# Kernel tuning notes

Hardware: AMD Instinct MI355X
Metric: run time of the kernel (lower is better)

The kernel has to match this reference:

```python
import jax, jax.numpy as jnp
import numpy as np


def setup_inputs() -> dict:
    key = jax.random.key(0)
    k1, k2, k3, k4 = jax.random.split(key, 4)
    B, S, E, D = 8, 2048, 1024, 64
    return {
        "sequence": jax.random.normal(k1, (B, S, E), dtype=jnp.float32),
        "Wk": jax.random.normal(k2, (E, D), dtype=jnp.float32) * (E ** -0.5),
        "Wq": jax.random.normal(k3, (E, D), dtype=jnp.float32) * (E ** -0.5),
        "Wv": jax.random.normal(k4, (E, D), dtype=jnp.float32) * (E ** -0.5),
    }


def reference(sequence, Wk, Wq, Wv):
    # sequence: [B, S, E]; Wk/Wq/Wv: [E, D]
    B, S, E = sequence.shape
    D = Wk.shape[-1]
    k = sequence @ Wk  # [B, S, D]
    q = sequence @ Wq  # [B, S, D]
    v = sequence @ Wv  # [B, S, D]
    scores = jnp.einsum("bqd,bkd->bqk", q, k) * (D ** -0.5)  # [B, S, S]
    causal = jnp.tril(jnp.ones((S, S), dtype=bool))
    scores = jnp.where(causal, scores, -jnp.inf)
    attn = jax.nn.softmax(scores, axis=-1)  # [B, S, S]
    out = jnp.einsum("bqk,bkd->bqd", attn, v)  # [B, S, D]
    return (out, attn)
```

## Files before the change

### kernel.cpp

```cpp
#include <hip/hip_runtime.h>
#include <hip/hip_bf16.h>


typedef __attribute__((ext_vector_type(8))) __bf16 bf16x8;
typedef __attribute__((ext_vector_type(4))) float f32x4;

constexpr int S_LEN = 2048;

__device__ inline unsigned short f2bf(float f) {
  union { float f; unsigned u; } v; v.f = f;
  unsigned u = v.u + 0x7FFFu + ((v.u >> 16) & 1u);
  return (unsigned short)(u >> 16);
}

__device__ inline uint4 pack8u(float4 f0, float4 f1) {
  union { __hip_bfloat162 h[4]; uint4 v; } u;
  u.h[0] = __float22bfloat162_rn(float2{f0.x, f0.y});
  u.h[1] = __float22bfloat162_rn(float2{f0.z, f0.w});
  u.h[2] = __float22bfloat162_rn(float2{f1.x, f1.y});
  u.h[3] = __float22bfloat162_rn(float2{f1.z, f1.w});
  return u.v;
}

__global__ __launch_bounds__(256) void wt_conv(
    const float* __restrict__ Wq, const float* __restrict__ Wk,
    const float* __restrict__ Wv, unsigned short* __restrict__ wt) {
  __shared__ float T[64][65];
  const int mat = blockIdx.y;
  const int k0 = blockIdx.x * 64;
  const float* W = (mat == 0) ? Wq : ((mat == 1) ? Wk : Wv);
  const int t = threadIdx.x;

  for (int s = 0; s < 4; ++s) {
    int rr = (t >> 4) + s * 16;
    int cc = (t & 15) * 4;
    float4 f = *(const float4*)(W + (size_t)(k0 + rr) * 64 + cc);
    T[rr][cc] = f.x; T[rr][cc + 1] = f.y; T[rr][cc + 2] = f.z; T[rr][cc + 3] = f.w;
  }
  __syncthreads();
  const float sc = (mat == 0) ? 0.125f : 1.0f;
  const int n = t >> 2, kc = (t & 3) * 16;
  union { unsigned short s[16]; uint4 v[2]; } tmp;
  for (int i = 0; i < 16; ++i) tmp.s[i] = f2bf(T[kc + i][n] * sc);
  unsigned short* dst = wt + (size_t)(mat * 64 + n) * 1024 + k0 + kc;
  *(uint4*)dst = tmp.v[0];
  *(uint4*)(dst + 8) = tmp.v[1];
}

__global__ __launch_bounds__(256) void qkv_gemm(
    const float* __restrict__ seq, const unsigned short* __restrict__ wt,
    unsigned short* __restrict__ qb, unsigned short* __restrict__ kb,
    unsigned short* __restrict__ vt) {
  __shared__ unsigned short As[64][72];
  const int row0 = blockIdx.x * 64;
  const int t = threadIdx.x;
  const int wv = t >> 6, lane = t & 63, lm = lane & 15, lq = lane >> 4;

  f32x4 acc[12];
  for (int i = 0; i < 12; ++i) acc[i] = (f32x4){0.f, 0.f, 0.f, 0.f};

  const int srow = t >> 2, skc = (t & 3) * 16;

  for (int i = 0; i < 16; ++i) {
    __syncthreads();
    const float* src = seq + (size_t)(row0 + srow) * 1024 + i * 64 + skc;
    float4 f0 = *(const float4*)src;
    float4 f1 = *(const float4*)(src + 4);
    float4 f2 = *(const float4*)(src + 8);
    float4 f3 = *(const float4*)(src + 12);
    *(uint4*)&As[srow][skc] = pack8u(f0, f1);
    *(uint4*)&As[srow][skc + 8] = pack8u(f2, f3);
    __syncthreads();
    for (int ks = 0; ks < 2; ++ks) {
      bf16x8 a[4];
      for (int mt = 0; mt < 4; ++mt)
        a[mt] = *(const bf16x8*)&As[mt * 16 + lm][ks * 32 + lq * 8];
      for (int nt = 0; nt < 3; ++nt) {
        const unsigned short* bp =
            wt + (size_t)(wv * 48 + nt * 16 + lm) * 1024 + i * 64 + ks * 32 + lq * 8;
        bf16x8 bfr = *(const bf16x8*)bp;
        for (int mt = 0; mt < 4; ++mt)
          acc[mt * 3 + nt] =
              __builtin_amdgcn_mfma_f32_16x16x32_bf16(a[mt], bfr, acc[mt * 3 + nt], 0, 0, 0);
      }
    }
  }

  const int bb = row0 >> 11;
  const int s0 = row0 & (S_LEN - 1);
  for (int nt = 0; nt < 3; ++nt) {
    int ng = wv * 48 + nt * 16 + lm;
    int mat = ng >> 6, d = ng & 63;
    for (int mt = 0; mt < 4; ++mt) {
      f32x4 v = acc[mt * 3 + nt];
      if (mat == 2) {
        ushort4 u;
        u.x = f2bf(v[0]); u.y = f2bf(v[1]); u.z = f2bf(v[2]); u.w = f2bf(v[3]);
        *(ushort4*)(vt + ((size_t)(bb * 64 + d)) * S_LEN + s0 + mt * 16 + lq * 4) = u;
      } else {
        unsigned short* dst = mat ? kb : qb;
        for (int r = 0; r < 4; ++r)
          dst[(size_t)(row0 + mt * 16 + lq * 4 + r) * 64 + d] = f2bf(v[r]);
      }
    }
  }
}

__global__ __launch_bounds__(256) void attn_stats(
    const unsigned short* __restrict__ qb, const unsigned short* __restrict__ kb,
    float* __restrict__ lbuf) {
  __shared__ unsigned short Ks[128][72];
  const int q0 = blockIdx.x * 64, c0 = blockIdx.y * 1024, b = blockIdx.z;
  if (c0 >= q0 + 64) return;
  const int kend = min(c0 + 1024, q0 + 64);
  const int t = threadIdx.x, wv = t >> 6, lane = t & 63, lm = lane & 15, lq = lane >> 4;

  const unsigned short* qp = qb + ((size_t)(b * S_LEN + q0 + wv * 16 + lm)) * 64 + lq * 8;
  bf16x8 qf0 = *(const bf16x8*)qp;
  bf16x8 qf1 = *(const bf16x8*)(qp + 32);
  const int rw0 = q0 + wv * 16;

  float lp[4] = {0.f, 0.f, 0.f, 0.f};
  const int srow = t >> 1, shalf = (t & 1) * 32;

  for (int kk = c0; kk < kend; kk += 128) {
    __syncthreads();
    const unsigned short* src = kb + ((size_t)(b * S_LEN + kk + srow)) * 64 + shalf;
    for (int j = 0; j < 4; ++j)
      *(uint4*)&Ks[srow][shalf + j * 8] = *(const uint4*)(src + j * 8);
    __syncthreads();
    if (kk <= rw0 + 15) {
      int ktmax = min(8, (rw0 + 15 - kk) / 16 + 1);
      for (int kt = 0; kt < ktmax; ++kt) {
        int key = kk + kt * 16 + lm;
        f32x4 z = (f32x4){0.f, 0.f, 0.f, 0.f};
        bf16x8 k0 = *(const bf16x8*)&Ks[kt * 16 + lm][lq * 8];
        bf16x8 k1 = *(const bf16x8*)&Ks[kt * 16 + lm][32 + lq * 8];
        z = __builtin_amdgcn_mfma_f32_16x16x32_bf16(qf0, k0, z, 0, 0, 0);
        z = __builtin_amdgcn_mfma_f32_16x16x32_bf16(qf1, k1, z, 0, 0, 0);
        for (int r = 0; r < 4; ++r) {
          float e = __expf(z[r]);
          lp[r] += (key <= rw0 + lq * 4 + r) ? e : 0.f;
        }
      }
    }
  }
  for (int off = 1; off < 16; off <<= 1)
    for (int r = 0; r < 4; ++r) lp[r] += __shfl_xor(lp[r], off);
  if (lm == 0)
    for (int r = 0; r < 4; ++r)
      unsafeAtomicAdd(&lbuf[b * S_LEN + rw0 + lq * 4 + r], lp[r]);
}

__global__ __launch_bounds__(256) void attn_write(
    const unsigned short* __restrict__ qb, const unsigned short* __restrict__ kb,
    const unsigned short* __restrict__ vt, const float* __restrict__ lbuf,
    float* __restrict__ outp, float* __restrict__ attnp) {
  __shared__ unsigned short Ks[256][72];
  __shared__ unsigned short Ps[4][16][72];
  const int q0 = blockIdx.x * 64, c0 = blockIdx.y * 256, b = blockIdx.z;
  const int t = threadIdx.x, wv = t >> 6, lane = t & 63, lm = lane & 15, lq = lane >> 4;
  float* arow = attnp + (size_t)b * S_LEN * S_LEN;

  if (c0 >= q0 + 64) {
    const int col = (t & 63) * 4, r0 = t >> 6;
    float4 z4 = {0.f, 0.f, 0.f, 0.f};
    for (int rr = r0; rr < 64; rr += 4)
      *(float4*)(arow + (size_t)(q0 + rr) * S_LEN + c0 + col) = z4;
    return;
  }

  {
    const unsigned short* src = kb + ((size_t)(b * S_LEN + c0 + t)) * 64;
    for (int j = 0; j < 8; ++j)
      *(uint4*)&Ks[t][j * 8] = *(const uint4*)(src + j * 8);
  }
  const unsigned short* qp = qb + ((size_t)(b * S_LEN + q0 + wv * 16 + lm)) * 64 + lq * 8;
  bf16x8 qf0 = *(const bf16x8*)qp;
  bf16x8 qf1 = *(const bf16x8*)(qp + 32);
  const int rw0 = q0 + wv * 16;

  float il[4];
  for (int r = 0; r < 4; ++r) il[r] = 1.0f / lbuf[b * S_LEN + rw0 + lq * 4 + r];

  f32x4 o[4];
  for (int i = 0; i < 4; ++i) o[i] = (f32x4){0.f, 0.f, 0.f, 0.f};
  __syncthreads();

  for (int st = 0; st < 4; ++st) {
    const int kk0 = c0 + st * 64;
    if (kk0 > rw0 + 15) {
      for (int rr = 0; rr < 16; ++rr)
        arow[(size_t)(rw0 + rr) * S_LEN + kk0 + lane] = 0.f;
      continue;
    }
    f32x4 c4[4];
    for (int kt = 0; kt < 4; ++kt) {
      f32x4 z = (f32x4){0.f, 0.f, 0.f, 0.f};
      bf16x8 k0 = *(const bf16x8*)&Ks[st * 64 + kt * 16 + lm][lq * 8];
      bf16x8 k1 = *(const bf16x8*)&Ks[st * 64 + kt * 16 + lm][32 + lq * 8];
      z = __builtin_amdgcn_mfma_f32_16x16x32_bf16(qf0, k0, z, 0, 0, 0);
      z = __builtin_amdgcn_mfma_f32_16x16x32_bf16(qf1, k1, z, 0, 0, 0);
      c4[kt] = z;
    }
    for (int kt = 0; kt < 4; ++kt) {
      int key = kk0 + kt * 16 + lm;
      for (int r = 0; r < 4; ++r) {
        int rw = rw0 + lq * 4 + r;
        float p = (key > rw) ? 0.f : __expf(c4[kt][r]) * il[r];
        arow[(size_t)rw * S_LEN + key] = p;
        Ps[wv][lq * 4 + r][kt * 16 + lm] = f2bf(p);
      }
    }
    for (int ks2 = 0; ks2 < 2; ++ks2) {
      bf16x8 pa = *(const bf16x8*)&Ps[wv][lm][ks2 * 32 + lq * 8];
      for (int nt = 0; nt < 4; ++nt) {
        const unsigned short* vp =
            vt + ((size_t)(b * 64 + nt * 16 + lm)) * S_LEN + kk0 + ks2 * 32 + lq * 8;
        o[nt] = __builtin_amdgcn_mfma_f32_16x16x32_bf16(pa, *(const bf16x8*)vp, o[nt], 0, 0, 0);
      }
    }
  }

  for (int nt = 0; nt < 4; ++nt)
    for (int r = 0; r < 4; ++r)
      unsafeAtomicAdd(outp + ((size_t)(b * S_LEN + rw0 + lq * 4 + r)) * 64 + nt * 16 + lm,
                      o[nt][r]);
}

extern "C" void kernel_launch(void* const* d_in, const int* in_sizes, int n_in,
                              void* d_out, int out_size, void* d_ws, size_t ws_size,
                              hipStream_t stream) {
  const float* seq = (const float*)d_in[0];
  const float* Wk  = (const float*)d_in[1];
  const float* Wq  = (const float*)d_in[2];
  const float* Wv  = (const float*)d_in[3];

  float* outp = (float*)d_out;
  float* attnp = outp + (size_t)8 * S_LEN * 64;

  unsigned short* qb = (unsigned short*)d_ws;
  unsigned short* kb = qb + (size_t)16384 * 64;
  unsigned short* vt = kb + (size_t)16384 * 64;
  unsigned short* wt = vt + (size_t)8 * 64 * S_LEN;
  float* lbuf = (float*)(wt + (size_t)192 * 1024);

  hipMemsetAsync(lbuf, 0, (size_t)16384 * 4, stream);
  hipMemsetAsync(outp, 0, (size_t)8 * S_LEN * 64 * 4, stream);

  wt_conv<<<dim3(16, 3), 256, 0, stream>>>(Wq, Wk, Wv, wt);
  qkv_gemm<<<dim3(256, 1), 256, 0, stream>>>(seq, wt, qb, kb, vt);
  attn_stats<<<dim3(32, 2, 8), 256, 0, stream>>>(qb, kb, lbuf);
  attn_write<<<dim3(32, 8, 8), 256, 0, stream>>>(qb, kb, vt, lbuf, outp, attnp);
}
```

Before: 253.7 us.

## Vectorize attention writes, double-buffer QKV GEMM, and split kernels finer

The QKV projection kernel now processes 32-row tiles across twice as many blocks. Its shared-memory A tile is double-buffered with register prefetch of the next K-slice, which removes one barrier per iteration. The stats and write kernels now load K tiles coalesced, and the stats kernel splits the key range into more chunks for extra parallelism. The attention-matrix write stores float4 vectors read back from the bf16 P tile instead of scattered scalar fp32 stores, and V fragments are prefetched before the softmax. The attn output is now bf16-rounded, which slightly reduces its precision.

```diff
diff --git a/kernel.cpp b/kernel.cpp
--- a/kernel.cpp
+++ b/kernel.cpp
@@ -11,6 +11,10 @@
   union { float f; unsigned u; } v; v.f = f;
   unsigned u = v.u + 0x7FFFu + ((v.u >> 16) & 1u);
   return (unsigned short)(u >> 16);
+}
+__device__ inline float bf2f(unsigned short s) {
+  union { unsigned u; float f; } v; v.u = ((unsigned)s) << 16;
+  return v.f;
 }
 
 __device__ inline uint4 pack8u(float4 f0, float4 f1) {
@@ -51,39 +55,40 @@
     const float* __restrict__ seq, const unsigned short* __restrict__ wt,
     unsigned short* __restrict__ qb, unsigned short* __restrict__ kb,
     unsigned short* __restrict__ vt) {
-  __shared__ unsigned short As[64][72];
-  const int row0 = blockIdx.x * 64;
+  __shared__ unsigned short As[2][32][72];
+  const int row0 = blockIdx.x * 32;
   const int t = threadIdx.x;
   const int wv = t >> 6, lane = t & 63, lm = lane & 15, lq = lane >> 4;
 
-  f32x4 acc[12];
-  for (int i = 0; i < 12; ++i) acc[i] = (f32x4){0.f, 0.f, 0.f, 0.f};
-
-  const int srow = t >> 2, skc = (t & 3) * 16;
+  f32x4 acc[6];
+  for (int i = 0; i < 6; ++i) acc[i] = (f32x4){0.f, 0.f, 0.f, 0.f};
+
+  const int srow = t >> 3, skc = (t & 7) * 8;
+  const float* ap = seq + (size_t)(row0 + srow) * 1024 + skc;
+
+  float4 f0 = *(const float4*)ap;
+  float4 f1 = *(const float4*)(ap + 4);
+  *(uint4*)&As[0][srow][skc] = pack8u(f0, f1);
 
   for (int i = 0; i < 16; ++i) {
+    if (i < 15) {
+      f0 = *(const float4*)(ap + (i + 1) * 64);
+      f1 = *(const float4*)(ap + (i + 1) * 64 + 4);
+    }
     __syncthreads();
-    const float* src = seq + (size_t)(row0 + srow) * 1024 + i * 64 + skc;
-    float4 f0 = *(const float4*)src;
-    float4 f1 = *(const float4*)(src + 4);
-    float4 f2 = *(const float4*)(src + 8);
-    float4 f3 = *(const float4*)(src + 12);
-    *(uint4*)&As[srow][skc] = pack8u(f0, f1);
-    *(uint4*)&As[srow][skc + 8] = pack8u(f2, f3);
-    __syncthreads();
+    const int buf = i & 1;
     for (int ks = 0; ks < 2; ++ks) {
-      bf16x8 a[4];
-      for (int mt = 0; mt < 4; ++mt)
-        a[mt] = *(const bf16x8*)&As[mt * 16 + lm][ks * 32 + lq * 8];
+      bf16x8 a0 = *(const bf16x8*)&As[buf][lm][ks * 32 + lq * 8];
+      bf16x8 a1 = *(const bf16x8*)&As[buf][16 + lm][ks * 32 + lq * 8];
       for (int nt = 0; nt < 3; ++nt) {
         const unsigned short* bp =
             wt + (size_t)(wv * 48 + nt * 16 + lm) * 1024 + i * 64 + ks * 32 + lq * 8;
         bf16x8 bfr = *(const bf16x8*)bp;
-        for (int mt = 0; mt < 4; ++mt)
-          acc[mt * 3 + nt] =
-              __builtin_amdgcn_mfma_f32_16x16x32_bf16(a[mt], bfr, acc[mt * 3 + nt], 0, 0, 0);
-      }
-    }
+        acc[nt] = __builtin_amdgcn_mfma_f32_16x16x32_bf16(a0, bfr, acc[nt], 0, 0, 0);
+        acc[3 + nt] = __builtin_amdgcn_mfma_f32_16x16x32_bf16(a1, bfr, acc[3 + nt], 0, 0, 0);
+      }
+    }
+    if (i < 15) *(uint4*)&As[buf ^ 1][srow][skc] = pack8u(f0, f1);
   }
 
   const int bb = row0 >> 11;
@@ -91,7 +96,7 @@
   for (int nt = 0; nt < 3; ++nt) {
     int ng = wv * 48 + nt * 16 + lm;
     int mat = ng >> 6, d = ng & 63;
-    for (int mt = 0; mt < 4; ++mt) {
+    for (int mt = 0; mt < 2; ++mt) {
       f32x4 v = acc[mt * 3 + nt];
       if (mat == 2) {
         ushort4 u;
@@ -110,9 +115,9 @@
     const unsigned short* __restrict__ qb, const unsigned short* __restrict__ kb,
     float* __restrict__ lbuf) {
   __shared__ unsigned short Ks[128][72];
-  const int q0 = blockIdx.x * 64, c0 = blockIdx.y * 1024, b = blockIdx.z;
+  const int q0 = blockIdx.x * 64, c0 = blockIdx.y * 512, b = blockIdx.z;
   if (c0 >= q0 + 64) return;
-  const int kend = min(c0 + 1024, q0 + 64);
+  const int kend = min(c0 + 512, q0 + 64);
   const int t = threadIdx.x, wv = t >> 6, lane = t & 63, lm = lane & 15, lq = lane >> 4;
 
   const unsigned short* qp = qb + ((size_t)(b * S_LEN + q0 + wv * 16 + lm)) * 64 + lq * 8;
@@ -121,13 +126,13 @@
   const int rw0 = q0 + wv * 16;
 
   float lp[4] = {0.f, 0.f, 0.f, 0.f};
-  const int srow = t >> 1, shalf = (t & 1) * 32;
+  const int sr = t >> 3, sc = (t & 7) * 8;
 
   for (int kk = c0; kk < kend; kk += 128) {
     __syncthreads();
-    const unsigned short* src = kb + ((size_t)(b * S_LEN + kk + srow)) * 64 + shalf;
+    const unsigned short* src = kb + ((size_t)(b * S_LEN + kk)) * 64;
     for (int j = 0; j < 4; ++j)
-      *(uint4*)&Ks[srow][shalf + j * 8] = *(const uint4*)(src + j * 8);
+      *(uint4*)&Ks[j * 32 + sr][sc] = *(const uint4*)(src + (size_t)(j * 32 + sr) * 64 + sc);
     __syncthreads();
     if (kk <= rw0 + 15) {
       int ktmax = min(8, (rw0 + 15 - kk) / 16 + 1);
@@ -171,9 +176,10 @@
   }
 
   {
-    const unsigned short* src = kb + ((size_t)(b * S_LEN + c0 + t)) * 64;
+    const int sr = t >> 3, sc = (t & 7) * 8;
+    const unsigned short* src = kb + ((size_t)(b * S_LEN + c0)) * 64;
     for (int j = 0; j < 8; ++j)
-      *(uint4*)&Ks[t][j * 8] = *(const uint4*)(src + j * 8);
+      *(uint4*)&Ks[j * 32 + sr][sc] = *(const uint4*)(src + (size_t)(j * 32 + sr) * 64 + sc);
   }
   const unsigned short* qp = qb + ((size_t)(b * S_LEN + q0 + wv * 16 + lm)) * 64 + lq * 8;
   bf16x8 qf0 = *(const bf16x8*)qp;
@@ -190,8 +196,9 @@
   for (int st = 0; st < 4; ++st) {
     const int kk0 = c0 + st * 64;
     if (kk0 > rw0 + 15) {
-      for (int rr = 0; rr < 16; ++rr)
-        arow[(size_t)(rw0 + rr) * S_LEN + kk0 + lane] = 0.f;
+      float4 z4 = {0.f, 0.f, 0.f, 0.f};
+      for (int r4 = 0; r4 < 4; ++r4)
+        *(float4*)(arow + (size_t)(rw0 + r4 * 4 + lq) * S_LEN + kk0 + lm * 4) = z4;
       continue;
     }
     f32x4 c4[4];
@@ -203,22 +210,30 @@
       z = __builtin_amdgcn_mfma_f32_16x16x32_bf16(qf1, k1, z, 0, 0, 0);
       c4[kt] = z;
     }
+    bf16x8 vf[2][4];
+    for (int ks2 = 0; ks2 < 2; ++ks2)
+      for (int nt = 0; nt < 4; ++nt)
+        vf[ks2][nt] = *(const bf16x8*)(vt + ((size_t)(b * 64 + nt * 16 + lm)) * S_LEN +
+                                       kk0 + ks2 * 32 + lq * 8);
     for (int kt = 0; kt < 4; ++kt) {
       int key = kk0 + kt * 16 + lm;
       for (int r = 0; r < 4; ++r) {
         int rw = rw0 + lq * 4 + r;
         float p = (key > rw) ? 0.f : __expf(c4[kt][r]) * il[r];
-        arow[(size_t)rw * S_LEN + key] = p;
         Ps[wv][lq * 4 + r][kt * 16 + lm] = f2bf(p);
       }
     }
     for (int ks2 = 0; ks2 < 2; ++ks2) {
       bf16x8 pa = *(const bf16x8*)&Ps[wv][lm][ks2 * 32 + lq * 8];
-      for (int nt = 0; nt < 4; ++nt) {
-        const unsigned short* vp =
-            vt + ((size_t)(b * 64 + nt * 16 + lm)) * S_LEN + kk0 + ks2 * 32 + lq * 8;
-        o[nt] = __builtin_amdgcn_mfma_f32_16x16x32_bf16(pa, *(const bf16x8*)vp, o[nt], 0, 0, 0);
-      }
+      for (int nt = 0; nt < 4; ++nt)
+        o[nt] = __builtin_amdgcn_mfma_f32_16x16x32_bf16(pa, vf[ks2][nt], o[nt], 0, 0, 0);
+    }
+    for (int r4 = 0; r4 < 4; ++r4) {
+      int row2 = r4 * 4 + lq;
+      ushort4 u = *(const ushort4*)&Ps[wv][row2][lm * 4];
+      float4 f;
+      f.x = bf2f(u.x); f.y = bf2f(u.y); f.z = bf2f(u.z); f.w = bf2f(u.w);
+      *(float4*)(arow + (size_t)(rw0 + row2) * S_LEN + kk0 + lm * 4) = f;
     }
   }
 
@@ -249,7 +264,7 @@
   hipMemsetAsync(outp, 0, (size_t)8 * S_LEN * 64 * 4, stream);
 
   wt_conv<<<dim3(16, 3), 256, 0, stream>>>(Wq, Wk, Wv, wt);
-  qkv_gemm<<<dim3(256, 1), 256, 0, stream>>>(seq, wt, qb, kb, vt);
-  attn_stats<<<dim3(32, 2, 8), 256, 0, stream>>>(qb, kb, lbuf);
+  qkv_gemm<<<dim3(512, 1), 256, 0, stream>>>(seq, wt, qb, kb, vt);
+  attn_stats<<<dim3(32, 4, 8), 256, 0, stream>>>(qb, kb, lbuf);
   attn_write<<<dim3(32, 8, 8), 256, 0, stream>>>(qb, kb, vt, lbuf, outp, attnp);
 }
```

New measurement: 249.0 us. No clear change (-1.9%).
